# Kernel optimization log

Hardware: AMD Instinct MI355X
Metric: run time of the kernel (lower is better)

Reference implementation:

```python
import jax, jax.numpy as jnp
import numpy as np

B, CQ, CKV, H, W = 8, 128, 64, 64, 64
DIM = CQ // 8  # qk_reduction=8 -> 16


def conv1x1(x, w, b):
    # x: [B, Cin, H, W], w: [Cout, Cin], b: [Cout]
    return jnp.einsum('bchw,oc->bohw', x, w) + b[None, :, None, None]


def setup_inputs() -> dict:
    key = jax.random.key(0)
    ks = jax.random.split(key, 12)
    s = 0.05
    return {
        'x4q': jax.random.normal(ks[0], (B, CQ, H, W), jnp.float32),
        'x4kv': jax.random.normal(ks[1], (B, CKV, H, W), jnp.float32),
        'Wq': jax.random.normal(ks[2], (DIM, CQ), jnp.float32) * s,
        'bq': jax.random.normal(ks[3], (DIM,), jnp.float32) * s,
        'Wk': jax.random.normal(ks[4], (DIM, CKV), jnp.float32) * s,
        'bk': jax.random.normal(ks[5], (DIM,), jnp.float32) * s,
        'Wv': jax.random.normal(ks[6], (CQ, CKV), jnp.float32) * s,
        'bv': jax.random.normal(ks[7], (CQ,), jnp.float32) * s,
        'Wo': jax.random.normal(ks[8], (CQ, CQ), jnp.float32) * s,
        'bo': jax.random.normal(ks[9], (CQ,), jnp.float32) * s,
        'gamma': jax.random.normal(ks[10], (1,), jnp.float32) * s,
    }


def reference(x4q, x4kv, Wq, bq, Wk, bk, Wv, bv, Wo, bo, gamma):
    q = conv1x1(x4q, Wq, bq)    # [B, DIM, H, W]
    k = conv1x1(x4kv, Wk, bk)   # [B, DIM, H, W]
    v = conv1x1(x4kv, Wv, bv)   # [B, CQ,  H, W]
    b, dim, h_, w_ = q.shape
    n = h_ * w_
    qf = q.reshape(b, dim, n)
    kf = k.reshape(b, dim, n)
    vf = v.reshape(b, -1, n)
    # score[b, n_query, m_key] = q^T k, scaled by dim^-0.5
    score = jnp.einsum('bdn,bdm->bnm', qf, kf) * (float(dim) ** -0.5)
    attention = jax.nn.softmax(score, axis=2)          # over keys m
    hmat = jnp.einsum('bcm,bnm->bcn', vf, attention)   # bmm(v, att^T)
    hmap = hmat.reshape(b, -1, h_, w_)
    hmap = conv1x1(hmap, Wo, bo)
    return gamma * hmap + x4q
```

## Files before the change

kernel.cpp:

```cpp
#include <hip/hip_runtime.h>

#define NB 8
#define CQ 128
#define CKV 64
#define NPIX 4096
#define QDIM 16
#define KVBLK 128
#define NTI (NPIX / KVBLK)

typedef float f32x4 __attribute__((ext_vector_type(4)));
typedef float f32x16 __attribute__((ext_vector_type(16)));
typedef __bf16 bf16x8 __attribute__((ext_vector_type(8)));
typedef unsigned short u16;
typedef u16 u16x4 __attribute__((ext_vector_type(4)));
typedef unsigned int u32;
typedef u32 u32x2 __attribute__((ext_vector_type(2)));
typedef u32 u32x4 __attribute__((ext_vector_type(4)));

static __device__ __forceinline__ u16 f2bf(float f) {
  unsigned int u = __builtin_bit_cast(unsigned int, f);
  u = (u + 0x7FFFu + ((u >> 16) & 1u)) >> 16;
  return (u16)u;
}
static __device__ __forceinline__ u32 cvtpk(float lo, float hi) {
  u32 r; asm("v_cvt_pk_bf16_f32 %0, %1, %2" : "=v"(r) : "v"(lo), "v"(hi)); return r;
}
static __device__ __forceinline__ void plswap(u32& a, u32& b) {
#if __has_builtin(__builtin_amdgcn_permlane32_swap)
  u32x2 r = __builtin_amdgcn_permlane32_swap(a, b, false, false);
  a = r[0]; b = r[1];
#else
  asm volatile("v_permlane32_swap_b32 %0, %1" : "+v"(a), "+v"(b));
#endif
}
static __device__ __forceinline__ void gload_lds16(const void* g, void* l) {
  __builtin_amdgcn_global_load_lds((const __attribute__((address_space(1))) void*)g,
                                   (__attribute__((address_space(3))) void*)l, 16, 0, 0);
}

__global__ __launch_bounds__(256) void proj_qkv(
    const float* __restrict__ xq, const float* __restrict__ Wq, const float* __restrict__ bq,
    const float* __restrict__ xkv, const float* __restrict__ Wk, const float* __restrict__ bk,
    const float* __restrict__ Wv, const float* __restrict__ bv,
    u16* __restrict__ Qs, u16* __restrict__ Ks, u16* __restrict__ Vt)
{
  __shared__ __align__(16) char smem[50688];
  int t = threadIdx.x;
  if ((int)blockIdx.x < NB * 64) {
    int bid = (int)blockIdx.x;
    float (*wq)[CQ]        = (float(*)[CQ])smem;
    float (*wk)[CKV]       = (float(*)[CKV])(smem + 8192);
    float (*redq)[64][17]  = (float(*)[64][17])(smem + 12288);
    float (*redk)[64][17]  = (float(*)[64][17])(smem + 29696);
    for (int i = t; i < QDIM * CQ; i += 256) wq[i >> 7][i & 127] = Wq[i];
    for (int i = t; i < QDIM * CKV; i += 256) wk[i >> 6][i & 63] = Wk[i];
    __syncthreads();
    int b = bid >> 6;
    int n0 = (bid & 63) << 6;
    int px = t & 63, cg = t >> 6;
    int n = n0 + px;
    const float* xqp = xq + (size_t)b * CQ * NPIX + n;
    const float* xkp = xkv + (size_t)b * CKV * NPIX + n;
    float qa[QDIM], ka[QDIM];
    #pragma unroll
    for (int d = 0; d < QDIM; d++) { qa[d] = 0.f; ka[d] = 0.f; }
    int cq0 = cg * 32, ck0 = cg * 16;
    #pragma unroll 4
    for (int c = cq0; c < cq0 + 32; c++) {
      float x = xqp[(size_t)c * NPIX];
      #pragma unroll
      for (int d = 0; d < QDIM; d++) qa[d] = fmaf(wq[d][c], x, qa[d]);
    }
    #pragma unroll 4
    for (int c = ck0; c < ck0 + 16; c++) {
      float x = xkp[(size_t)c * NPIX];
      #pragma unroll
      for (int d = 0; d < QDIM; d++) ka[d] = fmaf(wk[d][c], x, ka[d]);
    }
    #pragma unroll
    for (int d = 0; d < QDIM; d++) { redq[cg][px][d] = qa[d]; redk[cg][px][d] = ka[d]; }
    __syncthreads();
    const float SC = 0.25f * 1.44269504088896340736f;
    int d0 = cg * 4;
    u16x4 oq, ok;
    #pragma unroll
    for (int j = 0; j < 4; j++) {
      float sq = redq[0][px][d0 + j] + redq[1][px][d0 + j]
               + redq[2][px][d0 + j] + redq[3][px][d0 + j] + bq[d0 + j];
      oq[j] = f2bf(sq * SC);
      float sk = redk[0][px][d0 + j] + redk[1][px][d0 + j]
               + redk[2][px][d0 + j] + redk[3][px][d0 + j] + bk[d0 + j];
      ok[j] = f2bf(sk);
    }
    size_t o = ((size_t)b * NPIX + n) * QDIM + d0;
    *(u16x4*)(Qs + o) = oq;
    *(u16x4*)(Ks + o) = ok;
  } else {
    int bid = (int)blockIdx.x - NB * 64;
    float (*wv)[CKV + 1] = (float(*)[CKV + 1])smem;
    float (*xs)[64 + 4]  = (float(*)[64 + 4])(smem + 33280);
    int b = bid >> 6;
    int n0 = (bid & 63) << 6;
    for (int i = t; i < CQ * CKV; i += 256) wv[i >> 6][i & 63] = Wv[i];
    const float* xp = xkv + (size_t)b * CKV * NPIX + n0;
    for (int i = t; i < CKV * 16; i += 256) {
      int c = i >> 4, c4 = (i & 15) * 4;
      *(f32x4*)(&xs[c][c4]) = *(const f32x4*)(xp + (size_t)c * NPIX + c4);
    }
    __syncthreads();
    int cog = t >> 4, pg = t & 15;
    int co0 = cog * 8, p0 = pg * 4;
    float acc[8][4];
    #pragma unroll
    for (int j = 0; j < 8; j++) {
      float bb = bv[co0 + j];
      #pragma unroll
      for (int p = 0; p < 4; p++) acc[j][p] = bb;
    }
    #pragma unroll 2
    for (int c = 0; c < CKV; c++) {
      float xv[4];
      #pragma unroll
      for (int p = 0; p < 4; p++) xv[p] = xs[c][p0 + p];
      #pragma unroll
      for (int j = 0; j < 8; j++) {
        float wvv = wv[co0 + j][c];
        #pragma unroll
        for (int p = 0; p < 4; p++) acc[j][p] = fmaf(wvv, xv[p], acc[j][p]);
      }
    }
    #pragma unroll
    for (int j = 0; j < 8; j++) {
      u16x4 ov;
      #pragma unroll
      for (int p = 0; p < 4; p++) ov[p] = f2bf(acc[j][p]);
      *(u16x4*)(Vt + ((size_t)b * CQ + co0 + j) * NPIX + n0 + p0) = ov;
    }
  }
}

__global__ __launch_bounds__(512, 4) void attn(
    const u16* __restrict__ Qs, const u16* __restrict__ Ks, const u16* __restrict__ Vt,
    const float* __restrict__ Wo, const float* __restrict__ bo,
    const float* __restrict__ gamma, const float* __restrict__ xq,
    float* __restrict__ out)
{
  __shared__ u16 v_s[2][128][128];
  __shared__ float d_red[2][2][32];
  __shared__ float d_inv[2][32];
  __shared__ float bos[128];

  int t = (int)threadIdx.x;
  int w = t >> 6, l = t & 63, l31 = l & 31, hi = l >> 5;
  int p = w >> 2, ph = w & 3;
  int sw = ((int)blockIdx.x & 7) * 64 + ((int)blockIdx.x >> 3);
  int b = sw >> 6, q0 = (sw & 63) * 64;

  const u16* Qb = Qs + (size_t)b * NPIX * QDIM;
  const u16* Kb = Ks + (size_t)b * NPIX * QDIM;
  const u16* Vb = Vt + (size_t)b * CQ * NPIX;

  if (t < 128) bos[t] = bo[t];

  bf16x8 qf = *(const bf16x8*)(Qb + (size_t)(q0 + p * 32 + l31) * QDIM + hi * 8);

  int row0 = w * 16 + (l >> 4);
  int lx = (l & 15) ^ (l >> 4);
  const u16* kp = Kb + (size_t)(ph * 32 + l31) * QDIM + hi * 8;
  int rsw = l31 & 15;

  f32x16 acc[4];
  #pragma unroll
  for (int cb = 0; cb < 4; cb++)
    #pragma unroll
    for (int r = 0; r < 16; r++) acc[cb][r] = 0.f;
  float lsum = 0.f;

  f32x16 z;
  #pragma unroll
  for (int r = 0; r < 16; r++) z[r] = 0.f;

  #pragma unroll
  for (int j = 0; j < 4; j++)
    gload_lds16(Vb + (size_t)(row0 + j * 4) * NPIX + (lx ^ (j << 2)) * 8,
                &v_s[0][w * 16 + j * 4][0]);
  bf16x8 kc = *(const bf16x8*)(kp);
  bf16x8 kn = *(const bf16x8*)(kp + (size_t)KVBLK * QDIM);

  #pragma unroll 1
  for (int it = 0; it < NTI; it++) {
    __syncthreads();

    if (it + 1 < NTI) {
      #pragma unroll
      for (int j = 0; j < 4; j++)
        gload_lds16(Vb + (size_t)(row0 + j * 4) * NPIX + (lx ^ (j << 2)) * 8
                       + (size_t)(it + 1) * KVBLK,
                    &v_s[(it + 1) & 1][w * 16 + j * 4][0]);
    }

    f32x16 s = __builtin_amdgcn_mfma_f32_32x32x16_bf16(kc, qf, z, 0, 0, 0);
    kc = kn;
    if (it + 2 < NTI) kn = *(const bf16x8*)(kp + (size_t)(it + 2) * KVBLK * QDIM);

    float pv[16];
    #pragma unroll
    for (int r = 0; r < 16; r++) {
      pv[r] = __builtin_amdgcn_exp2f(s[r]);
      lsum += pv[r];
    }
    u32 a0 = cvtpk(pv[0], pv[1]),  b0 = cvtpk(pv[2], pv[3]);
    u32 c0 = cvtpk(pv[4], pv[5]),  d0 = cvtpk(pv[6], pv[7]);
    plswap(a0, c0); plswap(b0, d0);
    u32 a1 = cvtpk(pv[8], pv[9]),  b1 = cvtpk(pv[10], pv[11]);
    u32 c1 = cvtpk(pv[12], pv[13]), d1 = cvtpk(pv[14], pv[15]);
    plswap(a1, c1); plswap(b1, d1);
    u32x4 afw[2] = { {a0, b0, c0, d0}, {a1, b1, c1, d1} };

    const u16 (*vs)[128] = v_s[it & 1];
    #pragma unroll
    for (int c = 0; c < 2; c++) {
      bf16x8 af = __builtin_bit_cast(bf16x8, afw[c]);
      #pragma unroll
      for (int cb = 0; cb < 4; cb++) {
        int chunk = (ph * 4 + c * 2 + hi) ^ rsw;
        bf16x8 vf = *(const bf16x8*)(&vs[cb * 32 + l31][chunk * 8]);
        acc[cb] = __builtin_amdgcn_mfma_f32_32x32x16_bf16(af, vf, acc[cb], 0, 0, 0);
      }
    }
  }

  float tot = lsum + __shfl_xor(lsum, 32);
  __syncthreads();
  float* red = (float*)v_s;
  if (ph >= 2) {
    if (hi == 0) d_red[p][ph - 2][l31] = tot;
    float* dst = red + (((size_t)p * 2 + (ph - 2)) * 32) * 128;
    #pragma unroll
    for (int cb = 0; cb < 4; cb++)
      #pragma unroll
      for (int r = 0; r < 16; r++) {
        int row = (r & 3) + 8 * (r >> 2) + 4 * hi;
        dst[(size_t)row * 128 + cb * 32 + l31] = acc[cb][r];
      }
  }
  __syncthreads();
  if (ph < 2) {
    tot += d_red[p][ph][l31];
    const float* src = red + (((size_t)p * 2 + ph) * 32) * 128;
    #pragma unroll
    for (int cb = 0; cb < 4; cb++)
      #pragma unroll
      for (int r = 0; r < 16; r++) {
        int row = (r & 3) + 8 * (r >> 2) + 4 * hi;
        acc[cb][r] += src[(size_t)row * 128 + cb * 32 + l31];
      }
  }
  __syncthreads();
  if (ph == 1) {
    if (hi == 0) d_red[p][0][l31] = tot;
    float* dst = red + ((size_t)p * 2 * 32) * 128;
    #pragma unroll
    for (int cb = 0; cb < 4; cb++)
      #pragma unroll
      for (int r = 0; r < 16; r++) {
        int row = (r & 3) + 8 * (r >> 2) + 4 * hi;
        dst[(size_t)row * 128 + cb * 32 + l31] = acc[cb][r];
      }
  }
  __syncthreads();
  if (ph == 0) {
    tot += d_red[p][0][l31];
    if (hi == 0) d_inv[p][l31] = 1.0f / tot;
    const float* src = red + ((size_t)p * 2 * 32) * 128;
    #pragma unroll
    for (int cb = 0; cb < 4; cb++)
      #pragma unroll
      for (int r = 0; r < 16; r++) {
        int row = (r & 3) + 8 * (r >> 2) + 4 * hi;
        acc[cb][r] += src[(size_t)row * 128 + cb * 32 + l31];
      }
  }
  __syncthreads();
  u16* Old = (u16*)v_s;
  if (ph == 0) {
    #pragma unroll
    for (int cb = 0; cb < 4; cb++)
      #pragma unroll
      for (int r = 0; r < 16; r++) {
        int row = (r & 3) + 8 * (r >> 2) + 4 * hi;
        int q = p * 32 + row;
        int c = cb * 32 + l31;
        Old[q * 128 + (((c >> 3) ^ (row & 15)) << 3) + (c & 7)] =
            f2bf(acc[cb][r] * d_inv[p][row]);
      }
  }
  __syncthreads();
  int g2 = w >> 1, qh = w & 1;
  bf16x8 woF[8];
  {
    const float* wrow = Wo + (size_t)(g2 * 32 + l31) * CQ + hi * 8;
    #pragma unroll
    for (int kc8 = 0; kc8 < 8; kc8++) {
      f32x4 a = *(const f32x4*)(wrow + kc8 * 16);
      f32x4 c4 = *(const f32x4*)(wrow + kc8 * 16 + 4);
      u32x4 pk = { cvtpk(a[0], a[1]), cvtpk(a[2], a[3]),
                   cvtpk(c4[0], c4[1]), cvtpk(c4[2], c4[3]) };
      woF[kc8] = __builtin_bit_cast(bf16x8, pk);
    }
  }
  float g = gamma[0];
  const float* xb = xq + (size_t)b * CQ * NPIX;
  float* ob = out + (size_t)b * CQ * NPIX;
  f32x16 e = z;
  int q = qh * 32 + l31;
  #pragma unroll
  for (int kc8 = 0; kc8 < 8; kc8++) {
    int phys = (kc8 * 2 + hi) ^ (l31 & 15);
    bf16x8 of = *(const bf16x8*)(Old + q * 128 + phys * 8);
    e = __builtin_amdgcn_mfma_f32_32x32x16_bf16(woF[kc8], of, e, 0, 0, 0);
  }
  #pragma unroll
  for (int r = 0; r < 16; r++) {
    int o = g2 * 32 + (r & 3) + 8 * (r >> 2) + 4 * hi;
    size_t idx = (size_t)o * NPIX + q0 + qh * 32 + l31;
    ob[idx] = g * (e[r] + bos[o]) + xb[idx];
  }
}

extern "C" void kernel_launch(void* const* d_in, const int* in_sizes, int n_in,
                              void* d_out, int out_size, void* d_ws, size_t ws_size,
                              hipStream_t stream) {
  const float* x4q  = (const float*)d_in[0];
  const float* x4kv = (const float*)d_in[1];
  const float* Wq   = (const float*)d_in[2];
  const float* bq   = (const float*)d_in[3];
  const float* Wk   = (const float*)d_in[4];
  const float* bk   = (const float*)d_in[5];
  const float* Wv   = (const float*)d_in[6];
  const float* bv   = (const float*)d_in[7];
  const float* Wo   = (const float*)d_in[8];
  const float* bo   = (const float*)d_in[9];
  const float* gamma = (const float*)d_in[10];
  float* out = (float*)d_out;

  u16* Qs = (u16*)d_ws;
  u16* Ks = Qs + (size_t)NB * NPIX * QDIM;
  u16* Vt = Ks + (size_t)NB * NPIX * QDIM;

  proj_qkv<<<dim3(NB * 128), dim3(256), 0, stream>>>(x4q, Wq, bq, x4kv, Wk, bk,
                                                     Wv, bv, Qs, Ks, Vt);
  attn<<<dim3(NB * 64), dim3(512), 0, stream>>>(Qs, Ks, Vt, Wo, bo, gamma, x4q, out);
}
```

Measured before the change: 80.99 us.

## Double KV block size to 256 and hoist V fragment loads before softmax

Grows the per-iteration key/value tile from 128 to 256 pixels, so each warp computes two score MFMAs and feeds four P·V MFMA groups per iteration, halving the loop trip count and the number of barriers. V fragments are all loaded from LDS into registers up front so LDS latency overlaps the score MFMA and exp work. The V staging layout and XOR swizzle are rewritten for 256-wide rows. LDS doubles to 128KB and launch bounds drop to 2 blocks per SM, which trades occupancy and register pressure for fewer synchronisations.

```diff
diff --git a/kernel.cpp b/kernel.cpp
--- a/kernel.cpp
+++ b/kernel.cpp
@@ -5,7 +5,7 @@
 #define CKV 64
 #define NPIX 4096
 #define QDIM 16
-#define KVBLK 128
+#define KVBLK 256
 #define NTI (NPIX / KVBLK)
 
 typedef float f32x4 __attribute__((ext_vector_type(4)));
@@ -139,13 +139,13 @@
   }
 }
 
-__global__ __launch_bounds__(512, 4) void attn(
+__global__ __launch_bounds__(512, 2) void attn(
     const u16* __restrict__ Qs, const u16* __restrict__ Ks, const u16* __restrict__ Vt,
     const float* __restrict__ Wo, const float* __restrict__ bo,
     const float* __restrict__ gamma, const float* __restrict__ xq,
     float* __restrict__ out)
 {
-  __shared__ u16 v_s[2][128][128];
+  __shared__ u16 v_s[2][128][256];
   __shared__ float d_red[2][2][32];
   __shared__ float d_inv[2][32];
   __shared__ float bos[128];
@@ -164,9 +164,8 @@
 
   bf16x8 qf = *(const bf16x8*)(Qb + (size_t)(q0 + p * 32 + l31) * QDIM + hi * 8);
 
-  int row0 = w * 16 + (l >> 4);
-  int lx = (l & 15) ^ (l >> 4);
-  const u16* kp = Kb + (size_t)(ph * 32 + l31) * QDIM + hi * 8;
+  int l5 = l >> 5, c32 = l & 31;
+  const u16* kp = Kb + (size_t)(ph * 64 + l31) * QDIM + hi * 8;
   int rsw = l31 & 15;
 
   f32x16 acc[4];
@@ -180,12 +179,31 @@
   #pragma unroll
   for (int r = 0; r < 16; r++) z[r] = 0.f;
 
-  #pragma unroll
-  for (int j = 0; j < 4; j++)
-    gload_lds16(Vb + (size_t)(row0 + j * 4) * NPIX + (lx ^ (j << 2)) * 8,
-                &v_s[0][w * 16 + j * 4][0]);
-  bf16x8 kc = *(const bf16x8*)(kp);
-  bf16x8 kn = *(const bf16x8*)(kp + (size_t)KVBLK * QDIM);
+  auto PACK = [&](const f32x16& s, u32x4* aw) {
+    float pv[16];
+    #pragma unroll
+    for (int r = 0; r < 16; r++) {
+      pv[r] = __builtin_amdgcn_exp2f(s[r]);
+      lsum += pv[r];
+    }
+    u32 a0 = cvtpk(pv[0], pv[1]),  b0 = cvtpk(pv[2], pv[3]);
+    u32 c0 = cvtpk(pv[4], pv[5]),  d0 = cvtpk(pv[6], pv[7]);
+    plswap(a0, c0); plswap(b0, d0);
+    aw[0] = u32x4{a0, b0, c0, d0};
+    u32 a1 = cvtpk(pv[8], pv[9]),  b1 = cvtpk(pv[10], pv[11]);
+    u32 c1 = cvtpk(pv[12], pv[13]), d1 = cvtpk(pv[14], pv[15]);
+    plswap(a1, c1); plswap(b1, d1);
+    aw[1] = u32x4{a1, b1, c1, d1};
+  };
+
+  #pragma unroll
+  for (int j = 0; j < 8; j++)
+    gload_lds16(Vb + (size_t)(w * 16 + 2 * j + l5) * NPIX + (c32 ^ (2 * j + l5)) * 8,
+                &v_s[0][w * 16 + 2 * j][0]);
+  bf16x8 kcA = *(const bf16x8*)(kp);
+  bf16x8 kcB = *(const bf16x8*)(kp + 32 * QDIM);
+  bf16x8 knA = *(const bf16x8*)(kp + (size_t)KVBLK * QDIM);
+  bf16x8 knB = *(const bf16x8*)(kp + (size_t)KVBLK * QDIM + 32 * QDIM);
 
   #pragma unroll 1
   for (int it = 0; it < NTI; it++) {
@@ -193,40 +211,39 @@
 
     if (it + 1 < NTI) {
       #pragma unroll
-      for (int j = 0; j < 4; j++)
-        gload_lds16(Vb + (size_t)(row0 + j * 4) * NPIX + (lx ^ (j << 2)) * 8
+      for (int j = 0; j < 8; j++)
+        gload_lds16(Vb + (size_t)(w * 16 + 2 * j + l5) * NPIX + (c32 ^ (2 * j + l5)) * 8
                        + (size_t)(it + 1) * KVBLK,
-                    &v_s[(it + 1) & 1][w * 16 + j * 4][0]);
-    }
-
-    f32x16 s = __builtin_amdgcn_mfma_f32_32x32x16_bf16(kc, qf, z, 0, 0, 0);
-    kc = kn;
-    if (it + 2 < NTI) kn = *(const bf16x8*)(kp + (size_t)(it + 2) * KVBLK * QDIM);
-
-    float pv[16];
-    #pragma unroll
-    for (int r = 0; r < 16; r++) {
-      pv[r] = __builtin_amdgcn_exp2f(s[r]);
-      lsum += pv[r];
-    }
-    u32 a0 = cvtpk(pv[0], pv[1]),  b0 = cvtpk(pv[2], pv[3]);
-    u32 c0 = cvtpk(pv[4], pv[5]),  d0 = cvtpk(pv[6], pv[7]);
-    plswap(a0, c0); plswap(b0, d0);
-    u32 a1 = cvtpk(pv[8], pv[9]),  b1 = cvtpk(pv[10], pv[11]);
-    u32 c1 = cvtpk(pv[12], pv[13]), d1 = cvtpk(pv[14], pv[15]);
-    plswap(a1, c1); plswap(b1, d1);
-    u32x4 afw[2] = { {a0, b0, c0, d0}, {a1, b1, c1, d1} };
-
-    const u16 (*vs)[128] = v_s[it & 1];
-    #pragma unroll
-    for (int c = 0; c < 2; c++) {
+                    &v_s[(it + 1) & 1][w * 16 + 2 * j][0]);
+    }
+
+    const u16 (*vs)[256] = v_s[it & 1];
+    bf16x8 vf[16];
+    #pragma unroll
+    for (int c = 0; c < 4; c++)
+      #pragma unroll
+      for (int cb = 0; cb < 4; cb++)
+        vf[c * 4 + cb] =
+            *(const bf16x8*)(&vs[cb * 32 + l31][((ph * 8 + c * 2 + hi) ^ rsw) * 8]);
+
+    f32x16 s0 = __builtin_amdgcn_mfma_f32_32x32x16_bf16(kcA, qf, z, 0, 0, 0);
+    f32x16 s1 = __builtin_amdgcn_mfma_f32_32x32x16_bf16(kcB, qf, z, 0, 0, 0);
+    kcA = knA; kcB = knB;
+    if (it + 2 < NTI) {
+      knA = *(const bf16x8*)(kp + (size_t)(it + 2) * KVBLK * QDIM);
+      knB = *(const bf16x8*)(kp + (size_t)(it + 2) * KVBLK * QDIM + 32 * QDIM);
+    }
+
+    u32x4 afw[4];
+    PACK(s0, &afw[0]);
+    PACK(s1, &afw[2]);
+
+    #pragma unroll
+    for (int c = 0; c < 4; c++) {
       bf16x8 af = __builtin_bit_cast(bf16x8, afw[c]);
       #pragma unroll
-      for (int cb = 0; cb < 4; cb++) {
-        int chunk = (ph * 4 + c * 2 + hi) ^ rsw;
-        bf16x8 vf = *(const bf16x8*)(&vs[cb * 32 + l31][chunk * 8]);
-        acc[cb] = __builtin_amdgcn_mfma_f32_32x32x16_bf16(af, vf, acc[cb], 0, 0, 0);
-      }
+      for (int cb = 0; cb < 4; cb++)
+        acc[cb] = __builtin_amdgcn_mfma_f32_32x32x16_bf16(af, vf[c * 4 + cb], acc[cb], 0, 0, 0);
     }
   }
 
```

New measurement: 92.30 us. +14.0%, slower.
